# Kernel tuning notes

Measured on AMD Instinct MI355X. Metric: run time of the kernel, lower is better.

Reference implementation:

```python
import jax, jax.numpy as jnp
import numpy as np

N = 16384          # total nodes (128 graphs x 128 ops)
G = 128            # number of graphs
NPG = N // G       # nodes per graph
DIN = 64           # op_input_dim
H = 64             # hidden_dim
BN_EPS = 1e-5


def setup_inputs() -> dict:
    key = jax.random.key(0)
    ks = jax.random.split(key, 16)
    x = jax.random.normal(ks[0], (N, DIN), dtype=jnp.float32)
    # sparse-ish 0/1 adjacency stored dense (as torch.mm path expects); add self-loops so degrees > 0
    u = jax.random.uniform(ks[1], (N, N), dtype=jnp.float32)
    adj = jnp.maximum((u < 0.004).astype(jnp.float32), jnp.eye(N, dtype=jnp.float32))
    # graph_pool: [G, N] average-pooling matrix (block rows of 1/NPG)
    rows = jnp.repeat(jnp.arange(G), NPG)
    graph_pool = jnp.zeros((G, N), jnp.float32).at[rows, jnp.arange(N)].set(1.0 / NPG)
    s = 0.05
    params = {}
    dims_in = [DIN, H]
    for l in range(2):
        d_in = dims_in[l]
        params[f"W1_{l}"] = jax.random.normal(ks[2 + 6 * l], (d_in, H), jnp.float32) * s
        params[f"b1_{l}"] = jnp.zeros((H,), jnp.float32)
        params[f"g1_{l}"] = jnp.ones((H,), jnp.float32)
        params[f"be1_{l}"] = jnp.zeros((H,), jnp.float32)
        params[f"W2_{l}"] = jax.random.normal(ks[3 + 6 * l], (H, H), jnp.float32) * s
        params[f"b2_{l}"] = jnp.zeros((H,), jnp.float32)
        params[f"g_{l}"] = jnp.ones((H,), jnp.float32)   # outer BN gamma
        params[f"be_{l}"] = jnp.zeros((H,), jnp.float32)  # outer BN beta
    return {"x": x, "adj": adj, "graph_pool": graph_pool, **params}


def _bn(h, g, b):
    # training-mode BatchNorm1d over node axis (biased var), eps=1e-5
    m = jnp.mean(h, axis=0)
    v = jnp.var(h, axis=0)
    return g * (h - m) * jax.lax.rsqrt(v + BN_EPS) + b


def _mlp(h, W1, b1, g1, be1, W2, b2):
    # 2-layer MLP: Linear -> BN -> ReLU -> Linear
    return jax.nn.relu(_bn(h @ W1 + b1, g1, be1)) @ W2 + b2


def reference(x, adj, graph_pool,
              W1_0, b1_0, g1_0, be1_0, W2_0, b2_0, g_0, be_0,
              W1_1, b1_1, g1_1, be1_1, W2_1, b2_1, g_1, be_1):
    deg = adj @ jnp.ones((adj.shape[0], 1), adj.dtype)  # [N,1]
    h = x
    layers = [
        (W1_0, b1_0, g1_0, be1_0, W2_0, b2_0, g_0, be_0),
        (W1_1, b1_1, g1_1, be1_1, W2_1, b2_1, g_1, be_1),
    ]
    for (W1, b1, g1, be1, W2, b2, g, be) in layers:
        pooled = (adj @ h) / deg                 # average neighbor aggregation
        pooled_rep = _mlp(pooled, W1, b1, g1, be1, W2, b2)
        h = jax.nn.relu(_bn(pooled_rep, g, be))
    h_nodes = h
    pooled_h = graph_pool @ h                    # [G, H] graph readout
    return (pooled_h, h_nodes)
```

## Files before the change

### kernel.cpp

```cpp
#include <hip/hip_runtime.h>
#include <hip/hip_bf16.h>
#include <stdint.h>

#define N_NODES 16384
#define GG      128
#define HD      64
#define MAXD    192
#define BN_EPS  1e-5f

typedef unsigned short u16;
typedef unsigned int   u32;
typedef unsigned long long u64;
typedef u32 u32x4 __attribute__((ext_vector_type(4)));

__device__ __forceinline__ float bf2f(u16 u) {
    union { u32 i; float f; } c; c.i = ((u32)u) << 16; return c.f;
}
__device__ __forceinline__ float ldp(const void* p, int i, int flag) {
    return flag ? ((const float*)p)[i] : bf2f(((const u16*)p)[i]);
}

__global__ __launch_bounds__(256) void k_init(
    const u32* __restrict__ adj32, double* __restrict__ statsD,
    int* __restrict__ flag)
{
    const int gid = blockIdx.x * 256 + threadIdx.x;
    if (gid < 512) statsD[gid] = 0.0;
    if (gid == 0) *flag = ((adj32[0] & 0xFFFFu) == 0) ? 1 : 0;
}

__global__ __launch_bounds__(256) void k_scan(
    const void* __restrict__ adjv, u16* __restrict__ cols,
    int* __restrict__ cnt, const int* __restrict__ flagp)
{
    const int wave = threadIdx.x >> 6, lane = threadIdx.x & 63;
    const int row = blockIdx.x * 4 + wave;
    u16* __restrict__ crow = cols + (size_t)row * MAXD;
    const int flag = *flagp;
    const u64 ltmask = ((1ull << lane) - 1ull);

    int base = 0;
    if (flag) {
        const u32x4* __restrict__ arow =
            (const u32x4*)((const u32*)adjv + (size_t)row * N_NODES) + lane;
        u32x4 p0 = __builtin_nontemporal_load(arow);
        u32x4 p1 = __builtin_nontemporal_load(arow + 64);
        for (int c = 0; c < N_NODES; c += 256) {
            u32x4 raw = p0;
            p0 = p1;
            if (c + 512 < N_NODES)
                p1 = __builtin_nontemporal_load(arow + (c + 512) / 4);
            #pragma unroll
            for (int e = 0; e < 4; ++e) {
                u32 w = raw[e];
                u64 m = __ballot(w != 0);
                if (m) {
                    if (w) {
                        int p = base + __popcll(m & ltmask);
                        if (p < MAXD) crow[p] = (u16)(c + lane * 4 + e);
                    }
                    base += __popcll(m);
                }
            }
        }
    } else {
        const u32x4* __restrict__ arow =
            (const u32x4*)((const u16*)adjv + (size_t)row * N_NODES) + lane;
        u32x4 p0 = __builtin_nontemporal_load(arow);
        u32x4 p1 = __builtin_nontemporal_load(arow + 64);
        for (int c = 0; c < N_NODES; c += 512) {
            u32x4 raw = p0;
            p0 = p1;
            if (c + 1024 < N_NODES)
                p1 = __builtin_nontemporal_load(arow + (c + 1024) / 8);
            #pragma unroll
            for (int e = 0; e < 8; ++e) {
                u16 u = (u16)(raw[e >> 1] >> ((e & 1) * 16));
                u64 m = __ballot(u != 0);
                if (m) {
                    if (u) {
                        int p = base + __popcll(m & ltmask);
                        if (p < MAXD) crow[p] = (u16)(c + lane * 8 + e);
                    }
                    base += __popcll(m);
                }
            }
        }
    }
    if (lane == 0) cnt[row] = (base < MAXD) ? base : MAXD;
}

__global__ __launch_bounds__(256) void k_gather(
    const void* __restrict__ xv, const u16* __restrict__ cols,
    const int* __restrict__ cnt, float* __restrict__ invdeg,
    float* __restrict__ pooled, const int* __restrict__ flagp)
{
    const int wave = threadIdx.x >> 6, lane = threadIdx.x & 63;
    const int row = blockIdx.x * 4 + wave;
    const int flag = *flagp;
    const u16* __restrict__ crow = cols + (size_t)row * MAXD;
    const int n = cnt[row];
    float acc = 0.f;
    int k = 0;
    if (flag) {
        const float* __restrict__ x = (const float*)xv;
        for (; k + 4 <= n; k += 4) {
            ushort4 j4 = *(const ushort4*)&crow[k];
            float v0 = x[(size_t)j4.x * HD + lane];
            float v1 = x[(size_t)j4.y * HD + lane];
            float v2 = x[(size_t)j4.z * HD + lane];
            float v3 = x[(size_t)j4.w * HD + lane];
            acc += (v0 + v1) + (v2 + v3);
        }
        for (; k < n; ++k) acc += x[(size_t)crow[k] * HD + lane];
    } else {
        const u16* __restrict__ x = (const u16*)xv;
        for (; k + 4 <= n; k += 4) {
            ushort4 j4 = *(const ushort4*)&crow[k];
            float v0 = bf2f(x[(size_t)j4.x * HD + lane]);
            float v1 = bf2f(x[(size_t)j4.y * HD + lane]);
            float v2 = bf2f(x[(size_t)j4.z * HD + lane]);
            float v3 = bf2f(x[(size_t)j4.w * HD + lane]);
            acc += (v0 + v1) + (v2 + v3);
        }
        for (; k < n; ++k) acc += bf2f(x[(size_t)crow[k] * HD + lane]);
    }
    float inv = 1.f / (float)n;
    pooled[(size_t)row * HD + lane] = acc * inv;
    if (lane == 0) invdeg[row] = inv;
}

template<bool AFFINE>
__global__ __launch_bounds__(256) void k_mm(
    const float* __restrict__ src, const double* __restrict__ stats,
    const void* __restrict__ g, const void* __restrict__ be,
    const void* __restrict__ W, const void* __restrict__ bias,
    float* __restrict__ dst, const int* __restrict__ flagp)
{
    __shared__ float Wf[64 * 64];
    __shared__ float S[4 * 64];
    __shared__ float ac[128];
    const int tid = threadIdx.x;
    const int flag = *flagp;
    if (AFFINE) {
        if (tid < 64) {
            double m = stats[tid] * (1.0 / N_NODES);
            double v = stats[64 + tid] * (1.0 / N_NODES) - m * m;
            float A = ldp(g, tid, flag) / sqrtf((float)v + BN_EPS);
            ac[tid] = A;
            ac[64 + tid] = ldp(be, tid, flag) - (float)m * A;
        }
        __syncthreads();
    }
    for (int i = tid; i < 64 * 64; i += 256) Wf[i] = ldp(W, i, flag);
    const int rbase = blockIdx.x * 4;
    {
        float v = src[(size_t)rbase * 64 + tid];
        if (AFFINE) v = fmaxf(fmaf(ac[tid & 63], v, ac[64 + (tid & 63)]), 0.f);
        S[tid] = v;
    }
    __syncthreads();
    const int f = tid & 63, r = tid >> 6;
    float acc = ldp(bias, f, flag);
    #pragma unroll
    for (int k = 0; k < 64; ++k)
        acc = fmaf(S[r * 64 + k], Wf[k * 64 + f], acc);
    dst[(size_t)(rbase + r) * 64 + f] = acc;
}

__global__ __launch_bounds__(256) void k_stats(
    const float* __restrict__ src, double* __restrict__ statsOut)
{
    __shared__ double shs[256];
    __shared__ double shq[256];
    const int tid = threadIdx.x;
    const int f = tid & 63, rsub = tid >> 6;
    const int rbase = blockIdx.x * 64;
    double s = 0.0, q = 0.0;
    for (int r = rsub; r < 64; r += 4) {
        float v = src[(size_t)(rbase + r) * 64 + f];
        s += (double)v;
        q += (double)v * (double)v;
    }
    shs[tid] = s; shq[tid] = q;
    __syncthreads();
    if (tid < 64) {
        double S = shs[tid] + shs[64 + tid] + shs[128 + tid] + shs[192 + tid];
        double Q = shq[tid] + shq[64 + tid] + shq[128 + tid] + shq[192 + tid];
        atomicAdd(&statsOut[tid], S);
        atomicAdd(&statsOut[64 + tid], Q);
    }
}

__global__ __launch_bounds__(256) void k_bnrelu(
    const float* __restrict__ src, const double* __restrict__ stats,
    const void* __restrict__ g, const void* __restrict__ be,
    float* __restrict__ dst, const int* __restrict__ flagp)
{
    __shared__ float ac[128];
    const int tid = threadIdx.x;
    const int flag = *flagp;
    if (tid < 64) {
        double m = stats[tid] * (1.0 / N_NODES);
        double v = stats[64 + tid] * (1.0 / N_NODES) - m * m;
        float A = ldp(g, tid, flag) / sqrtf((float)v + BN_EPS);
        ac[tid] = A;
        ac[64 + tid] = ldp(be, tid, flag) - (float)m * A;
    }
    __syncthreads();
    const size_t idx = ((size_t)blockIdx.x * 256 + tid) * 4;
    const int f0 = (int)(idx & 63);
    float4 t = *(const float4*)&src[idx];
    const float4 A4 = *(const float4*)&ac[f0];
    const float4 C4 = *(const float4*)&ac[64 + f0];
    float4 r;
    r.x = fmaxf(fmaf(A4.x, t.x, C4.x), 0.f);
    r.y = fmaxf(fmaf(A4.y, t.y, C4.y), 0.f);
    r.z = fmaxf(fmaf(A4.z, t.z, C4.z), 0.f);
    r.w = fmaxf(fmaf(A4.w, t.w, C4.w), 0.f);
    *(float4*)&dst[idx] = r;
}

__global__ __launch_bounds__(256) void k_spmm(
    const float* __restrict__ t, const double* __restrict__ stats,
    const void* __restrict__ g, const void* __restrict__ be,
    const u16* __restrict__ cols, const int* __restrict__ cnt,
    const float* __restrict__ invdeg, float* __restrict__ pooled,
    const int* __restrict__ flagp)
{
    const int wave = threadIdx.x >> 6, lane = threadIdx.x & 63;
    const int row = blockIdx.x * 4 + wave;
    const int flag = *flagp;
    double md = stats[lane] * (1.0 / N_NODES);
    double vd = stats[64 + lane] * (1.0 / N_NODES) - md * md;
    const float A = ldp(g, lane, flag) / sqrtf((float)vd + BN_EPS);
    const float C = ldp(be, lane, flag) - (float)md * A;

    const u16* __restrict__ crow = cols + (size_t)row * MAXD;
    const int n = cnt[row];
    float acc = 0.f;
    int k = 0;
    for (; k + 4 <= n; k += 4) {
        ushort4 j4 = *(const ushort4*)&crow[k];
        float v0 = t[(size_t)j4.x * HD + lane];
        float v1 = t[(size_t)j4.y * HD + lane];
        float v2 = t[(size_t)j4.z * HD + lane];
        float v3 = t[(size_t)j4.w * HD + lane];
        acc += fmaxf(fmaf(A, v0, C), 0.f);
        acc += fmaxf(fmaf(A, v1, C), 0.f);
        acc += fmaxf(fmaf(A, v2, C), 0.f);
        acc += fmaxf(fmaf(A, v3, C), 0.f);
    }
    for (; k < n; ++k) {
        float vv = t[(size_t)crow[k] * HD + lane];
        acc += fmaxf(fmaf(A, vv, C), 0.f);
    }
    pooled[(size_t)row * HD + lane] = acc * invdeg[row];
}

__global__ __launch_bounds__(1024) void k_pool(
    const void* __restrict__ gpv, const float* __restrict__ h,
    float* __restrict__ out, const int* __restrict__ flagp)
{
    __shared__ float red[16 * 64];
    const int g = blockIdx.x;
    const int wave = threadIdx.x >> 6, lane = threadIdx.x & 63;
    const int flag = *flagp;
    float acc = 0.f;
    const int jb0 = wave * (N_NODES / 16);
    if (flag) {
        const float* __restrict__ grow = (const float*)gpv + (size_t)g * N_NODES;
        for (int jb = jb0; jb < jb0 + N_NODES / 16; jb += 4) {
            float4 raw = *(const float4*)(grow + jb);
            if (raw.x != 0.f) acc += raw.x * h[(size_t)(jb + 0) * HD + lane];
            if (raw.y != 0.f) acc += raw.y * h[(size_t)(jb + 1) * HD + lane];
            if (raw.z != 0.f) acc += raw.z * h[(size_t)(jb + 2) * HD + lane];
            if (raw.w != 0.f) acc += raw.w * h[(size_t)(jb + 3) * HD + lane];
        }
    } else {
        const u16* __restrict__ grow = (const u16*)gpv + (size_t)g * N_NODES;
        for (int jb = jb0; jb < jb0 + N_NODES / 16; jb += 8) {
            uint4 raw = *(const uint4*)(grow + jb);
            const u32 w[4] = {raw.x, raw.y, raw.z, raw.w};
            #pragma unroll
            for (int e = 0; e < 8; ++e) {
                u16 u = (u16)(w[e >> 1] >> ((e & 1) * 16));
                if (u) acc += bf2f(u) * h[(size_t)(jb + e) * HD + lane];
            }
        }
    }
    red[wave * 64 + lane] = acc;
    __syncthreads();
    if (wave == 0) {
        float s = 0.f;
        #pragma unroll
        for (int w2 = 0; w2 < 16; ++w2) s += red[w2 * 64 + lane];
        out[g * 64 + lane] = s;
    }
}

extern "C" void kernel_launch(void* const* d_in, const int* in_sizes, int n_in,
                              void* d_out, int out_size, void* d_ws, size_t ws_size,
                              hipStream_t stream)
{
    const void* x    = d_in[0];
    const void* adj  = d_in[1];
    const void* gp   = d_in[2];
    const void* W1_0 = d_in[3];
    const void* b1_0 = d_in[4];
    const void* g1_0 = d_in[5];
    const void* be1_0= d_in[6];
    const void* W2_0 = d_in[7];
    const void* b2_0 = d_in[8];
    const void* g_0  = d_in[9];
    const void* be_0 = d_in[10];
    const void* W1_1 = d_in[11];
    const void* b1_1 = d_in[12];
    const void* g1_1 = d_in[13];
    const void* be1_1= d_in[14];
    const void* W2_1 = d_in[15];
    const void* b2_1 = d_in[16];
    const void* g_1  = d_in[17];
    const void* be_1 = d_in[18];

    char* ws = (char*)d_ws;
    float*  P      = (float*) (ws);
    float*  A      = (float*) (ws + (4u  << 20));
    float*  B      = (float*) (ws + (8u  << 20));
    u16*    cols   = (u16*)   (ws + (12u << 20));
    int*    cnt    = (int*)   (ws + (18u << 20));
    float*  invdeg = (float*) (ws + (18u << 20) + 65536);
    double* sd     = (double*)(ws + (18u << 20) + 131072);
    int*    flag   = (int*)   (ws + (18u << 20) + 131072 + 4096);

    float* out_pool  = (float*)d_out;
    float* out_nodes = (float*)d_out + GG * HD;

    const int EB = (N_NODES * HD / 4) / 256;

    k_init<<<2, 256, 0, stream>>>((const u32*)adj, sd, flag);
    k_scan<<<N_NODES / 4, 256, 0, stream>>>(adj, cols, cnt, flag);
    k_gather<<<N_NODES / 4, 256, 0, stream>>>(x, cols, cnt, invdeg, P, flag);

    k_mm<false><<<N_NODES / 4, 256, 0, stream>>>(P, nullptr, nullptr, nullptr,
                                                 W1_0, b1_0, A, flag);
    k_stats<<<256, 256, 0, stream>>>(A, sd + 0);
    k_mm<true><<<N_NODES / 4, 256, 0, stream>>>(A, sd + 0, g1_0, be1_0,
                                                W2_0, b2_0, P, flag);
    k_stats<<<256, 256, 0, stream>>>(P, sd + 128);
    k_spmm<<<N_NODES / 4, 256, 0, stream>>>(P, sd + 128, g_0, be_0,
                                            cols, cnt, invdeg, B, flag);
    k_mm<false><<<N_NODES / 4, 256, 0, stream>>>(B, nullptr, nullptr, nullptr,
                                                 W1_1, b1_1, A, flag);
    k_stats<<<256, 256, 0, stream>>>(A, sd + 256);
    k_mm<true><<<N_NODES / 4, 256, 0, stream>>>(A, sd + 256, g1_1, be1_1,
                                                W2_1, b2_1, P, flag);
    k_stats<<<256, 256, 0, stream>>>(P, sd + 384);
    k_bnrelu<<<EB, 256, 0, stream>>>(P, sd + 384, g_1, be_1, out_nodes, flag);
    k_pool<<<GG, 1024, 0, stream>>>(gp, out_nodes, out_pool, flag);
}
```

Before: 1.626 ms.

## Fuse adjacency scan with gather and tile dense matmul over 16 rows

Merges the init, adjacency-scan and first neighbor-gather kernels into one kernel that stages column indices in shared memory and gathers from there, while still writing them to global memory for the later spmm. The dense 64x64 matmul kernel now handles 16 rows per block with 4 accumulators per thread, so each block loads W once for four times as many rows. This cuts two launches, the global round-trip of the index lists, and repeated weight loads. The flag is now recomputed in each block from adj, and the stats zeroing moves into the fused kernel.

```diff
diff --git a/kernel.cpp b/kernel.cpp
--- a/kernel.cpp
+++ b/kernel.cpp
@@ -20,25 +20,24 @@
     return flag ? ((const float*)p)[i] : bf2f(((const u16*)p)[i]);
 }
 
-__global__ __launch_bounds__(256) void k_init(
-    const u32* __restrict__ adj32, double* __restrict__ statsD,
-    int* __restrict__ flag)
-{
+__global__ __launch_bounds__(256) void k_scan_gather(
+    const void* __restrict__ adjv, const void* __restrict__ xv,
+    u16* __restrict__ cols, int* __restrict__ cnt,
+    float* __restrict__ invdeg, float* __restrict__ pooled,
+    double* __restrict__ statsD, int* __restrict__ flagp)
+{
+    __shared__ __align__(16) u16 sc[4][MAXD];
+    const int wave = threadIdx.x >> 6, lane = threadIdx.x & 63;
+    const int row = blockIdx.x * 4 + wave;
+    const u32 w0 = *(const u32*)adjv;
+    const int flag = ((w0 & 0xFFFFu) == 0) ? 1 : 0;
+    const u64 ltmask = ((1ull << lane) - 1ull);
+
     const int gid = blockIdx.x * 256 + threadIdx.x;
     if (gid < 512) statsD[gid] = 0.0;
-    if (gid == 0) *flag = ((adj32[0] & 0xFFFFu) == 0) ? 1 : 0;
-}
-
-__global__ __launch_bounds__(256) void k_scan(
-    const void* __restrict__ adjv, u16* __restrict__ cols,
-    int* __restrict__ cnt, const int* __restrict__ flagp)
-{
-    const int wave = threadIdx.x >> 6, lane = threadIdx.x & 63;
-    const int row = blockIdx.x * 4 + wave;
-    u16* __restrict__ crow = cols + (size_t)row * MAXD;
-    const int flag = *flagp;
-    const u64 ltmask = ((1ull << lane) - 1ull);
-
+    if (gid == 0) *flagp = flag;
+
+    u16* __restrict__ srow = sc[wave];
     int base = 0;
     if (flag) {
         const u32x4* __restrict__ arow =
@@ -57,7 +56,7 @@
                 if (m) {
                     if (w) {
                         int p = base + __popcll(m & ltmask);
-                        if (p < MAXD) crow[p] = (u16)(c + lane * 4 + e);
+                        if (p < MAXD) srow[p] = (u16)(c + lane * 4 + e);
                     }
                     base += __popcll(m);
                 }
@@ -80,50 +79,48 @@
                 if (m) {
                     if (u) {
                         int p = base + __popcll(m & ltmask);
-                        if (p < MAXD) crow[p] = (u16)(c + lane * 8 + e);
+                        if (p < MAXD) srow[p] = (u16)(c + lane * 8 + e);
                     }
                     base += __popcll(m);
                 }
             }
         }
     }
-    if (lane == 0) cnt[row] = (base < MAXD) ? base : MAXD;
-}
-
-__global__ __launch_bounds__(256) void k_gather(
-    const void* __restrict__ xv, const u16* __restrict__ cols,
-    const int* __restrict__ cnt, float* __restrict__ invdeg,
-    float* __restrict__ pooled, const int* __restrict__ flagp)
-{
-    const int wave = threadIdx.x >> 6, lane = threadIdx.x & 63;
-    const int row = blockIdx.x * 4 + wave;
-    const int flag = *flagp;
-    const u16* __restrict__ crow = cols + (size_t)row * MAXD;
-    const int n = cnt[row];
+    const int n = (base < MAXD) ? base : MAXD;
+    if (lane == 0) cnt[row] = n;
+    __syncthreads();
+
+    {
+        u32* __restrict__ crow32 = (u32*)(cols + (size_t)row * MAXD);
+        const u32* __restrict__ s32 = (const u32*)srow;
+        #pragma unroll
+        for (int t = lane; t < MAXD / 2; t += 64) crow32[t] = s32[t];
+    }
+
     float acc = 0.f;
     int k = 0;
     if (flag) {
         const float* __restrict__ x = (const float*)xv;
         for (; k + 4 <= n; k += 4) {
-            ushort4 j4 = *(const ushort4*)&crow[k];
+            ushort4 j4 = *(const ushort4*)&srow[k];
             float v0 = x[(size_t)j4.x * HD + lane];
             float v1 = x[(size_t)j4.y * HD + lane];
             float v2 = x[(size_t)j4.z * HD + lane];
             float v3 = x[(size_t)j4.w * HD + lane];
             acc += (v0 + v1) + (v2 + v3);
         }
-        for (; k < n; ++k) acc += x[(size_t)crow[k] * HD + lane];
+        for (; k < n; ++k) acc += x[(size_t)srow[k] * HD + lane];
     } else {
         const u16* __restrict__ x = (const u16*)xv;
         for (; k + 4 <= n; k += 4) {
-            ushort4 j4 = *(const ushort4*)&crow[k];
+            ushort4 j4 = *(const ushort4*)&srow[k];
             float v0 = bf2f(x[(size_t)j4.x * HD + lane]);
             float v1 = bf2f(x[(size_t)j4.y * HD + lane]);
             float v2 = bf2f(x[(size_t)j4.z * HD + lane]);
             float v3 = bf2f(x[(size_t)j4.w * HD + lane]);
             acc += (v0 + v1) + (v2 + v3);
         }
-        for (; k < n; ++k) acc += bf2f(x[(size_t)crow[k] * HD + lane]);
+        for (; k < n; ++k) acc += bf2f(x[(size_t)srow[k] * HD + lane]);
     }
     float inv = 1.f / (float)n;
     pooled[(size_t)row * HD + lane] = acc * inv;
@@ -138,7 +135,7 @@
     float* __restrict__ dst, const int* __restrict__ flagp)
 {
     __shared__ float Wf[64 * 64];
-    __shared__ float S[4 * 64];
+    __shared__ float S[16 * 64];
     __shared__ float ac[128];
     const int tid = threadIdx.x;
     const int flag = *flagp;
@@ -153,19 +150,34 @@
         __syncthreads();
     }
     for (int i = tid; i < 64 * 64; i += 256) Wf[i] = ldp(W, i, flag);
-    const int rbase = blockIdx.x * 4;
+    const int rbase = blockIdx.x * 16;
     {
-        float v = src[(size_t)rbase * 64 + tid];
-        if (AFFINE) v = fmaxf(fmaf(ac[tid & 63], v, ac[64 + (tid & 63)]), 0.f);
-        S[tid] = v;
-    }
-    __syncthreads();
-    const int f = tid & 63, r = tid >> 6;
-    float acc = ldp(bias, f, flag);
+        float4 v = *(const float4*)&src[(size_t)rbase * 64 + tid * 4];
+        if (AFFINE) {
+            const int f0 = (tid * 4) & 63;
+            v.x = fmaxf(fmaf(ac[f0 + 0], v.x, ac[64 + f0 + 0]), 0.f);
+            v.y = fmaxf(fmaf(ac[f0 + 1], v.y, ac[64 + f0 + 1]), 0.f);
+            v.z = fmaxf(fmaf(ac[f0 + 2], v.z, ac[64 + f0 + 2]), 0.f);
+            v.w = fmaxf(fmaf(ac[f0 + 3], v.w, ac[64 + f0 + 3]), 0.f);
+        }
+        *(float4*)&S[tid * 4] = v;
+    }
+    __syncthreads();
+    const int f = tid & 63, r0 = (tid >> 6) * 4;
+    const float b = ldp(bias, f, flag);
+    float a0 = b, a1 = b, a2 = b, a3 = b;
     #pragma unroll
-    for (int k = 0; k < 64; ++k)
-        acc = fmaf(S[r * 64 + k], Wf[k * 64 + f], acc);
-    dst[(size_t)(rbase + r) * 64 + f] = acc;
+    for (int k = 0; k < 64; ++k) {
+        const float wk = Wf[k * 64 + f];
+        a0 = fmaf(S[(r0 + 0) * 64 + k], wk, a0);
+        a1 = fmaf(S[(r0 + 1) * 64 + k], wk, a1);
+        a2 = fmaf(S[(r0 + 2) * 64 + k], wk, a2);
+        a3 = fmaf(S[(r0 + 3) * 64 + k], wk, a3);
+    }
+    dst[(size_t)(rbase + r0 + 0) * 64 + f] = a0;
+    dst[(size_t)(rbase + r0 + 1) * 64 + f] = a1;
+    dst[(size_t)(rbase + r0 + 2) * 64 + f] = a2;
+    dst[(size_t)(rbase + r0 + 3) * 64 + f] = a3;
 }
 
 __global__ __launch_bounds__(256) void k_stats(
@@ -338,23 +350,22 @@
 
     const int EB = (N_NODES * HD / 4) / 256;
 
-    k_init<<<2, 256, 0, stream>>>((const u32*)adj, sd, flag);
-    k_scan<<<N_NODES / 4, 256, 0, stream>>>(adj, cols, cnt, flag);
-    k_gather<<<N_NODES / 4, 256, 0, stream>>>(x, cols, cnt, invdeg, P, flag);
-
-    k_mm<false><<<N_NODES / 4, 256, 0, stream>>>(P, nullptr, nullptr, nullptr,
-                                                 W1_0, b1_0, A, flag);
+    k_scan_gather<<<N_NODES / 4, 256, 0, stream>>>(adj, x, cols, cnt,
+                                                   invdeg, P, sd, flag);
+
+    k_mm<false><<<N_NODES / 16, 256, 0, stream>>>(P, nullptr, nullptr, nullptr,
+                                                  W1_0, b1_0, A, flag);
     k_stats<<<256, 256, 0, stream>>>(A, sd + 0);
-    k_mm<true><<<N_NODES / 4, 256, 0, stream>>>(A, sd + 0, g1_0, be1_0,
-                                                W2_0, b2_0, P, flag);
+    k_mm<true><<<N_NODES / 16, 256, 0, stream>>>(A, sd + 0, g1_0, be1_0,
+                                                 W2_0, b2_0, P, flag);
     k_stats<<<256, 256, 0, stream>>>(P, sd + 128);
     k_spmm<<<N_NODES / 4, 256, 0, stream>>>(P, sd + 128, g_0, be_0,
                                             cols, cnt, invdeg, B, flag);
-    k_mm<false><<<N_NODES / 4, 256, 0, stream>>>(B, nullptr, nullptr, nullptr,
-                                                 W1_1, b1_1, A, flag);
+    k_mm<false><<<N_NODES / 16, 256, 0, stream>>>(B, nullptr, nullptr, nullptr,
+                                                  W1_1, b1_1, A, flag);
     k_stats<<<256, 256, 0, stream>>>(A, sd + 256);
-    k_mm<true><<<N_NODES / 4, 256, 0, stream>>>(A, sd + 256, g1_1, be1_1,
-                                                W2_1, b2_1, P, flag);
+    k_mm<true><<<N_NODES / 16, 256, 0, stream>>>(A, sd + 256, g1_1, be1_1,
+                                                 W2_1, b2_1, P, flag);
     k_stats<<<256, 256, 0, stream>>>(P, sd + 384);
     k_bnrelu<<<EB, 256, 0, stream>>>(P, sd + 384, g_1, be_1, out_nodes, flag);
     k_pool<<<GG, 1024, 0, stream>>>(gp, out_nodes, out_pool, flag);
```

New measurement: 1.604 ms. Within noise of the previous version (-1.4%).
